# Performance work log

Measured on AMD Instinct MI355X. Metric: run time of the kernel, lower is better.

## Reference

```python
import jax, jax.numpy as jnp
import numpy as np

H_SVD_MEDIUM_20 = np.array([+0.3279, +1.0, -0.9373, -0.8584, +0.6153, -0.5127, -0.3207, +0.8355,
                            -0.7528, +0.6792, +0.5284, -0.8558, -0.4101, -0.7967, -0.6088, -0.5275,
                            -0.2591, +0.894, +0.0663, +0.1645], dtype=np.float32)

def _inv_softplus(y, eps=1e-8):
    y = float(max(y, eps))
    return float(np.log(np.expm1(y)))

def setup_inputs() -> dict:
    key = jax.random.key(0)
    k1, k2, k3 = jax.random.split(key, 3)
    B, L, K, NUM_AA = 32, 8192, 64, 20
    seq = jax.random.randint(k1, (B, L), 0, NUM_AA, dtype=jnp.int64 if jax.config.jax_enable_x64 else jnp.int32)
    r = jax.random.uniform(k2, (B, L, K), dtype=jnp.float32) * 15.0
    j_idx = jax.random.randint(k3, (B, L, K), 0, L, dtype=seq.dtype)
    h = jnp.asarray(H_SVD_MEDIUM_20)                      # learned pair vector, SVD init
    r_half_raw = jnp.float32(_inv_softplus(6.5))
    tau_hp_raw = jnp.float32(_inv_softplus(1.5))
    return {"seq": seq, "r": r, "j_idx": j_idx, "h": h,
            "r_half_raw": r_half_raw, "tau_hp_raw": tau_hp_raw, "max_dist": 10}

def reference(seq, r, j_idx, h, r_half_raw, tau_hp_raw, max_dist):
    B, L, K = r.shape
    md = jnp.float32(max_dist)
    r_peak = jax.nn.softplus(r_half_raw)
    sigma = jax.nn.softplus(tau_hp_raw) + 0.1
    valid = (r < md - 1e-4).astype(r.dtype)               # [B,L,K]
    h_i = h[seq]                                          # [B,L]
    j_safe = jnp.clip(j_idx, 0, L - 1)
    seq_j = jnp.take_along_axis(seq, j_safe.reshape(B, L * K), axis=1).reshape(B, L, K)
    h_j = h[seq_j]                                        # [B,L,K]
    r_c = jnp.minimum(r, md)
    g = jnp.exp(-(r_c - r_peak) ** 2 / (2.0 * sigma ** 2)) * valid
    E_hp_i = jnp.sum(h_i[..., None] * h_j * g, axis=-1)   # [B,L]
    return E_hp_i
```

## Files before the change

kernel.cpp:

```cpp
#include <hip/hip_runtime.h>


#define BB 32
#define LL 8192
#define KK 64
#define TPB 1024
#define RPB 512
#define DEPTH 4

__device__ __forceinline__ float row16_sum(float x) {
    x += __int_as_float(__builtin_amdgcn_mov_dpp(__float_as_int(x), 0x111, 0xF, 0xF, true));
    x += __int_as_float(__builtin_amdgcn_mov_dpp(__float_as_int(x), 0x112, 0xF, 0xF, true));
    x += __int_as_float(__builtin_amdgcn_mov_dpp(__float_as_int(x), 0x114, 0xF, 0xF, true));
    x += __int_as_float(__builtin_amdgcn_mov_dpp(__float_as_int(x), 0x118, 0xF, 0xF, true));
    return x;
}

__global__ __launch_bounds__(TPB) void _HydrophobicPairs_58256936403302_kernel(
    const int*   __restrict__ seq,
    const float* __restrict__ r,
    const int*   __restrict__ j_idx,
    const float* __restrict__ h,
    const float* __restrict__ r_half_raw,
    const float* __restrict__ tau_hp_raw,
    const int*   __restrict__ max_dist,
    float*       __restrict__ out)
{
    __shared__ float h_row[LL];
    const int tid   = threadIdx.x;
    const int b     = blockIdx.x >> 4;
    const int chunk = blockIdx.x & 15;
    const int lbase = chunk * RPB;

    const int4* seq4 = (const int4*)(seq + b * LL);
    #pragma unroll
    for (int i = 0; i < 2; ++i) {
        const int e4 = i * TPB + tid;
        const int4 s = seq4[e4];
        ((float4*)h_row)[e4] = make_float4(h[s.x], h[s.y], h[s.z], h[s.w]);
    }

    const float md     = (float)max_dist[0];
    const float r_peak = log1pf(expf(r_half_raw[0]));
    const float sigma  = log1pf(expf(tau_hp_raw[0])) + 0.1f;
    const float nscale = -1.44269504f / (2.0f * sigma * sigma);
    const float c1     = -2.0f * nscale * r_peak;
    const float c0     = nscale * r_peak * r_peak;
    const float vthr   = md - 1e-4f;

    const int lane = tid & 15;
    const int rgrp = tid >> 4;
    const long base0 = ((long)(b * LL + lbase + rgrp)) * KK + lane * 4;

    float4 rbuf[DEPTH]; int4 jbuf[DEPTH];
    #pragma unroll
    for (int p = 0; p < DEPTH; ++p) {
        const long nb = base0 + (long)p * (64 * KK);
        rbuf[p] = *(const float4*)(r + nb);
        jbuf[p] = *(const int4*)(j_idx + nb);
    }

    __syncthreads();

    #pragma unroll
    for (int it = 0; it < 8; ++it) {
        const int slot = it & (DEPTH - 1);
        const float4 rc = rbuf[slot];
        const int4   jc = jbuf[slot];
        if (it + DEPTH < 8) {
            const long nb = base0 + (long)(it + DEPTH) * (64 * KK);
            rbuf[slot] = *(const float4*)(r + nb);
            jbuf[slot] = *(const int4*)(j_idx + nb);
        }

        float acc = 0.0f;
        #pragma unroll
        for (int u = 0; u < 4; ++u) {
            const float rv = (&rc.x)[u];
            const unsigned j = (unsigned)(&jc.x)[u] & (LL - 1);
            const float hj = h_row[j];
            const float uexp = fmaf(rv, fmaf(nscale, rv, c1), c0);
            float g = exp2f(uexp);
            g = (rv < vthr) ? g : 0.0f;
            acc = fmaf(hj, g, acc);
        }

        acc = row16_sum(acc);

        if (lane == 15) {
            const int l_loc = lbase + it * 64 + rgrp;
            out[b * LL + l_loc] = h_row[l_loc] * acc;
        }
    }
}

extern "C" void kernel_launch(void* const* d_in, const int* in_sizes, int n_in,
                              void* d_out, int out_size, void* d_ws, size_t ws_size,
                              hipStream_t stream) {
    const int*   seq        = (const int*)d_in[0];
    const float* r          = (const float*)d_in[1];
    const int*   j_idx      = (const int*)d_in[2];
    const float* h          = (const float*)d_in[3];
    const float* r_half_raw = (const float*)d_in[4];
    const float* tau_hp_raw = (const float*)d_in[5];
    const int*   max_dist   = (const int*)d_in[6];
    float*       out        = (float*)d_out;

    _HydrophobicPairs_58256936403302_kernel<<<dim3(BB * (LL / RPB)), dim3(TPB), 0, stream>>>(
        seq, r, j_idx, h, r_half_raw, tau_hp_raw, max_dist, out);
}
```

Measured before the change: 160.8 us.

## Stream r and j_idx through LDS with async global_load_lds double buffering

Halves the block size to 512 threads and gives each wave 64 contiguous rows. Those rows' r and j_idx tiles are streamed into per-wave LDS double buffers with global_load_lds DMA and manual vmcnt waits. The goal is to keep loads in flight without holding register-resident prefetch buffers, which should reduce VGPR pressure. In exchange it adds LDS traffic and manual waitcnt bookkeeping. That bookkeeping risks ordering bugs, and per-wave prefetch depth is only two chunks.

```diff
diff --git a/kernel.cpp b/kernel.cpp
--- a/kernel.cpp
+++ b/kernel.cpp
@@ -4,9 +4,16 @@
 #define BB 32
 #define LL 8192
 #define KK 64
-#define TPB 1024
+#define TPB 512
 #define RPB 512
-#define DEPTH 4
+#define NWAVE 8
+#define NCHUNK 16
+
+__device__ __forceinline__ void dma16(const void* g, void* l) {
+    __builtin_amdgcn_global_load_lds(
+        (const __attribute__((address_space(1))) void*)g,
+        (__attribute__((address_space(3))) void*)l, 16, 0, 0);
+}
 
 __device__ __forceinline__ float row16_sum(float x) {
     x += __int_as_float(__builtin_amdgcn_mov_dpp(__float_as_int(x), 0x111, 0xF, 0xF, true));
@@ -27,14 +34,17 @@
     float*       __restrict__ out)
 {
     __shared__ float h_row[LL];
-    const int tid   = threadIdx.x;
+    __shared__ __align__(16) char sbuf[NWAVE][2][2048];
+
+    const int tid  = threadIdx.x;
+    const int wave = tid >> 6;
+    const int lane = tid & 63;
     const int b     = blockIdx.x >> 4;
-    const int chunk = blockIdx.x & 15;
-    const int lbase = chunk * RPB;
+    const int lbase = (blockIdx.x & 15) * RPB;
 
     const int4* seq4 = (const int4*)(seq + b * LL);
     #pragma unroll
-    for (int i = 0; i < 2; ++i) {
+    for (int i = 0; i < 4; ++i) {
         const int e4 = i * TPB + tid;
         const int4 s = seq4[e4];
         ((float4*)h_row)[e4] = make_float4(h[s.x], h[s.y], h[s.z], h[s.w]);
@@ -48,29 +58,35 @@
     const float c0     = nscale * r_peak * r_peak;
     const float vthr   = md - 1e-4f;
 
-    const int lane = tid & 15;
-    const int rgrp = tid >> 4;
-    const long base0 = ((long)(b * LL + lbase + rgrp)) * KK + lane * 4;
-
-    float4 rbuf[DEPTH]; int4 jbuf[DEPTH];
-    #pragma unroll
-    for (int p = 0; p < DEPTH; ++p) {
-        const long nb = base0 + (long)p * (64 * KK);
-        rbuf[p] = *(const float4*)(r + nb);
-        jbuf[p] = *(const int4*)(j_idx + nb);
-    }
-
     __syncthreads();
 
+    const int l0 = lbase + wave * 64;
+    const char* rg = (const char*)(r     + (long)(b * LL + l0) * KK) + lane * 16;
+    const char* jg = (const char*)(j_idx + (long)(b * LL + l0) * KK) + lane * 16;
+
+    dma16(rg + 0 * 1024, &sbuf[wave][0][0]);
+    dma16(jg + 0 * 1024, &sbuf[wave][0][1024]);
+    dma16(rg + 1 * 1024, &sbuf[wave][1][0]);
+    dma16(jg + 1 * 1024, &sbuf[wave][1][1024]);
+
+    const int myrow = lane >> 4;
+    const int klane = lane & 15;
+
     #pragma unroll
-    for (int it = 0; it < 8; ++it) {
-        const int slot = it & (DEPTH - 1);
-        const float4 rc = rbuf[slot];
-        const int4   jc = jbuf[slot];
-        if (it + DEPTH < 8) {
-            const long nb = base0 + (long)(it + DEPTH) * (64 * KK);
-            rbuf[slot] = *(const float4*)(r + nb);
-            jbuf[slot] = *(const int4*)(j_idx + nb);
+    for (int c = 0; c < NCHUNK; ++c) {
+        if      (c == 0)          asm volatile("s_waitcnt vmcnt(2)" ::: "memory");
+        else if (c == 1)          asm volatile("s_waitcnt vmcnt(3)" ::: "memory");
+        else if (c == NCHUNK - 1) asm volatile("s_waitcnt vmcnt(2)" ::: "memory");
+        else                      asm volatile("s_waitcnt vmcnt(4)" ::: "memory");
+
+        const int slot = c & 1;
+        const float4 rc = *(const float4*)(&sbuf[wave][slot][lane * 16]);
+        const int4   jc = *(const int4*)(&sbuf[wave][slot][1024 + lane * 16]);
+        asm volatile("s_waitcnt lgkmcnt(0)" ::: "memory");
+
+        if (c + 2 < NCHUNK) {
+            dma16(rg + (c + 2) * 1024, &sbuf[wave][slot][0]);
+            dma16(jg + (c + 2) * 1024, &sbuf[wave][slot][1024]);
         }
 
         float acc = 0.0f;
@@ -87,9 +103,9 @@
 
         acc = row16_sum(acc);
 
-        if (lane == 15) {
-            const int l_loc = lbase + it * 64 + rgrp;
-            out[b * LL + l_loc] = h_row[l_loc] * acc;
+        if (klane == 15) {
+            const int lrow = l0 + c * 4 + myrow;
+            out[b * LL + lrow] = h_row[lrow] * acc;
         }
     }
 }
```

After: 158.7 us. Within noise of the previous version (-1.3%).
